# Kernel tuning notes

Hardware: AMD Instinct MI355X
Metric: run time of the kernel (lower is better)

Reference implementation:

```python
import jax, jax.numpy as jnp
import numpy as np

K = 512          # num_embeddings
D = 8            # latent_dim
DECAY = 0.99     # ema_decay
EPS = 1e-5


def setup_inputs() -> dict:
    key = jax.random.key(0)
    k1, k2 = jax.random.split(key)
    z = jax.random.normal(k1, (64, D, 64, 64), dtype=jnp.float32)
    # codebook initialized uniform(-1/K, 1/K) as in the torch module
    codebook = jax.random.uniform(k2, (K, D), dtype=jnp.float32,
                                  minval=-1.0 / K, maxval=1.0 / K)
    ema_cluster_size = jnp.zeros((K,), dtype=jnp.float32)
    ema_w = jnp.zeros((K, D), dtype=jnp.float32)
    return {"z": z, "codebook": codebook,
            "ema_cluster_size": ema_cluster_size, "ema_w": ema_w}


def reference(z, codebook, ema_cluster_size, ema_w):
    B, C, H, W = z.shape
    # (B, HW, C) flattened latents, matching z.view(B,C,-1).permute(0,2,1)
    flat = z.reshape(B, C, H * W).transpose(0, 2, 1)

    # cdist p=2: ||z||^2 - 2 z.e + ||e||^2, then sqrt (argmin unaffected,
    # but we keep the sqrt for faithfulness to torch.cdist)
    z_sq = jnp.sum(flat * flat, axis=-1, keepdims=True)        # (B, N, 1)
    e_sq = jnp.sum(codebook * codebook, axis=-1)               # (K,)
    dots = jnp.einsum('bnd,kd->bnk', flat, codebook)           # (B, N, K)
    distances = jnp.sqrt(jnp.maximum(z_sq - 2.0 * dots + e_sq, 0.0))

    indices = jnp.argmin(distances, axis=-1)                   # (B, N) int

    # embedding gather with the OLD codebook (as in the torch forward)
    z_q = codebook[indices]                                    # (B, N, D)
    z_q = z_q.transpose(0, 2, 1).reshape(B, C, H, W)

    commitment_loss = jnp.mean((jax.lax.stop_gradient(z_q) - z) ** 2)
    loss = commitment_loss  # use_ema=True branch

    # ---- EMA in-place codebook update (buffers) ----
    idx_flat = indices.reshape(-1)                             # (B*N,)
    inp_flat = flat.reshape(-1, C)                             # (B*N, D)
    counts = jax.ops.segment_sum(jnp.ones_like(idx_flat, dtype=z.dtype),
                                 idx_flat, num_segments=K)     # (K,)
    sums = jax.ops.segment_sum(inp_flat, idx_flat, num_segments=K)  # (K, D)

    new_cs = ema_cluster_size * DECAY + counts * (1.0 - DECAY)
    new_w = ema_w * DECAY + sums * (1.0 - DECAY)
    n = jnp.sum(new_cs)
    cs_smoothed = (new_cs + EPS) / (n + K * EPS) * n
    new_codebook = new_w / cs_smoothed[:, None]

    return z_q, loss, new_codebook, cs_smoothed, new_w
```

## Files before the change

kernel.cpp:

```cpp
#include <hip/hip_runtime.h>

constexpr int Kc   = 512;
constexpr int Dc   = 8;
constexpr int HWc  = 4096;
constexpr int CHWc = Dc * HWc;
constexpr int Mc   = 64 * HWc;
constexpr int TOTALc = Mc * Dc;

constexpr int REP      = 8;
constexpr int RSTRIDE  = 4616;
constexpr int ACC_FLOATS = REP * RSTRIDE;

typedef float v2f __attribute__((ext_vector_type(2)));

__global__ __launch_bounds__(256) void vq_prep(const float* __restrict__ cb,
                                               float* __restrict__ ws) {
    const int tid = blockIdx.x * 256 + threadIdx.x;
    float4* w4 = (float4*)ws;
    for (int i = tid; i < ACC_FLOATS / 4; i += gridDim.x * 256)
        w4[i] = float4{0.f, 0.f, 0.f, 0.f};
    if (blockIdx.x == 0) {
        for (int k = threadIdx.x; k < Kc; k += 256) {
            float s = 0.f;
#pragma unroll
            for (int c = 0; c < Dc; ++c) {
                const float e = cb[k * Dc + c];
                s = fmaf(e, e, s);
            }
            ws[ACC_FLOATS + k] = s;
        }
    }
}

__global__ __launch_bounds__(512, 8) void vq_main(const float* __restrict__ z,
                                                  const float* __restrict__ cb,
                                                  const float* __restrict__ esq,
                                                  float* __restrict__ ws,
                                                  float* __restrict__ zq) {
    __shared__ float s_mn[8][256];
    __shared__ int   s_im[8][256];
    __shared__ float s_counts[Kc];
    __shared__ float s_sums[Kc * Dc];
    __shared__ float s_loss;

    const int t = threadIdx.x;
    for (int i = t; i < Kc; i += 512) s_counts[i] = 0.f;
    for (int i = t; i < Kc * Dc; i += 512) s_sums[i] = 0.f;
    if (t == 0) s_loss = 0.f;

    const int l = t & 63;
    const int g  = __builtin_amdgcn_readfirstlane(t >> 6);
    const int k0 = g << 6;

    const int base = blockIdx.x * 256;
    const int b  = base >> 12;
    const int n0 = (base & (HWc - 1)) + l;
    const float* zb = z + b * CHWc + n0;

    v2f zzA[Dc], zzB[Dc];
#pragma unroll
    for (int c = 0; c < Dc; ++c) {
        zzA[c] = v2f{-2.0f * zb[c * HWc],       -2.0f * zb[c * HWc + 64]};
        zzB[c] = v2f{-2.0f * zb[c * HWc + 128], -2.0f * zb[c * HWc + 192]};
    }

    const unsigned long long* cbq = (const unsigned long long*)cb;

    float mn0 = 3.4e38f, mn1 = 3.4e38f, mn2 = 3.4e38f, mn3 = 3.4e38f;
    int   i0 = k0, i1 = k0, i2 = k0, i3 = k0;
#pragma unroll 2
    for (int kk = 0; kk < 64; ++kk) {
        const int k = k0 + kk;
        const unsigned long long q0 = cbq[4 * k + 0];
        const unsigned long long q1 = cbq[4 * k + 1];
        const unsigned long long q2 = cbq[4 * k + 2];
        const unsigned long long q3 = cbq[4 * k + 3];
        const float ev = esq[k];
        v2f aA = {ev, ev};
        v2f aB = {ev, ev};
#define PKSTEP(Q, P0, P1)                                              \
        asm("v_pk_fma_f32 %0, %2, %4, %0 op_sel_hi:[1,0,1]\n\t"        \
            "v_pk_fma_f32 %1, %3, %4, %1 op_sel_hi:[1,0,1]\n\t"        \
            "v_pk_fma_f32 %0, %5, %4, %0 op_sel:[0,1,0]\n\t"           \
            "v_pk_fma_f32 %1, %6, %4, %1 op_sel:[0,1,0]"               \
            : "+v"(aA), "+v"(aB)                                       \
            : "v"(zzA[P0]), "v"(zzB[P0]), "s"(Q), "v"(zzA[P1]), "v"(zzB[P1]))
        PKSTEP(q0, 0, 1);
        PKSTEP(q1, 2, 3);
        PKSTEP(q2, 4, 5);
        PKSTEP(q3, 6, 7);
#undef PKSTEP
        const float a0 = aA.x, a1 = aA.y, a2 = aB.x, a3 = aB.y;
        bool c;
        c = a0 < mn0; mn0 = c ? a0 : mn0; i0 = c ? k : i0;
        c = a1 < mn1; mn1 = c ? a1 : mn1; i1 = c ? k : i1;
        c = a2 < mn2; mn2 = c ? a2 : mn2; i2 = c ? k : i2;
        c = a3 < mn3; mn3 = c ? a3 : mn3; i3 = c ? k : i3;
    }
    s_mn[g][l]       = mn0;  s_im[g][l]       = i0;
    s_mn[g][l +  64] = mn1;  s_im[g][l +  64] = i1;
    s_mn[g][l + 128] = mn2;  s_im[g][l + 128] = i2;
    s_mn[g][l + 192] = mn3;  s_im[g][l + 192] = i3;
    __syncthreads();

    if (t < 256) {
        const int v = t;
        float mn = s_mn[0][v];
        int   im = s_im[0][v];
#pragma unroll
        for (int gg = 1; gg < 8; ++gg) {
            const float m2 = s_mn[gg][v];
            const int   j2 = s_im[gg][v];
            const bool  c2 = m2 < mn;
            mn = c2 ? m2 : mn;
            im = c2 ? j2 : im;
        }

        const float4* cb4 = (const float4*)cb;
        const float4 qa = cb4[im * 2], qb = cb4[im * 2 + 1];
        const float q[Dc] = {qa.x, qa.y, qa.z, qa.w, qb.x, qb.y, qb.z, qb.w};

        const int nv = (base & (HWc - 1)) + v;
        const float* zv = z + b * CHWc + nv;
        float* zqv = zq + b * CHWc + nv;
        float lsum = 0.f;
        float zr[Dc];
#pragma unroll
        for (int c = 0; c < Dc; ++c) {
            zr[c] = zv[c * HWc];
            zqv[c * HWc] = q[c];
            const float d = q[c] - zr[c];
            lsum = fmaf(d, d, lsum);
        }

        unsafeAtomicAdd(&s_counts[im], 1.0f);
#pragma unroll
        for (int c = 0; c < Dc; ++c)
            unsafeAtomicAdd(&s_sums[im * Dc + c], zr[c]);
        unsafeAtomicAdd(&s_loss, lsum);
    }
    __syncthreads();

    float* acc = ws + (blockIdx.x & (REP - 1)) * RSTRIDE;
    for (int i = t; i < Kc; i += 512) {
        const float val = s_counts[i];
        if (val != 0.f) unsafeAtomicAdd(&acc[i], val);
    }
    for (int i = t; i < Kc * Dc; i += 512) {
        const float val = s_sums[i];
        if (val != 0.f) unsafeAtomicAdd(&acc[512 + i], val);
    }
    if (t == 0) unsafeAtomicAdd(&acc[4608], s_loss);
}

__global__ __launch_bounds__(512) void vq_final(const float* __restrict__ ws,
                                                const float* __restrict__ ema_cs,
                                                const float* __restrict__ ema_w,
                                                float* __restrict__ out) {
    constexpr float DEC  = 0.99f;
    constexpr float OMD  = (float)(1.0 - 0.99);
    constexpr float EPSf = 1e-5f;
    constexpr float KEPS = (float)(512 * 1e-5);
    __shared__ float red[512];
    __shared__ float s_cs[512];

    const int t = threadIdx.x;
    float cnt = 0.f;
#pragma unroll
    for (int r = 0; r < REP; ++r) cnt += ws[r * RSTRIDE + t];
    const float ncs = ema_cs[t] * DEC + cnt * OMD;
    red[t] = ncs;
    __syncthreads();
    for (int s = 256; s > 0; s >>= 1) {
        if (t < s) red[t] += red[t + s];
        __syncthreads();
    }
    const float n  = red[0];
    const float cs = (ncs + EPSf) / (n + KEPS) * n;
    s_cs[t] = cs;

    float* out_loss = out + TOTALc;
    float* out_cb   = out + TOTALc + 1;
    float* out_cs   = out_cb + Kc * Dc;
    float* out_nw   = out_cs + Kc;

    __syncthreads();

    const int blk = blockIdx.x;
    if (blk == 0) {
        out_cs[t] = cs;
        if (t == 0) {
            float ls = 0.f;
#pragma unroll
            for (int r = 0; r < REP; ++r) ls += ws[r * RSTRIDE + 4608];
            out_loss[0] = ls * (1.0f / 2097152.0f);
        }
    } else {
        const int e = (blk - 1) * 512 + t;
        float sm = 0.f;
#pragma unroll
        for (int r = 0; r < REP; ++r) sm += ws[r * RSTRIDE + 512 + e];
        const float nw = ema_w[e] * DEC + sm * OMD;
        out_nw[e] = nw;
        out_cb[e] = nw / s_cs[e >> 3];
    }
}

extern "C" void kernel_launch(void* const* d_in, const int* in_sizes, int n_in,
                              void* d_out, int out_size, void* d_ws, size_t ws_size,
                              hipStream_t stream) {
    const float* z      = (const float*)d_in[0];
    const float* cb     = (const float*)d_in[1];
    const float* ema_cs = (const float*)d_in[2];
    const float* ema_w  = (const float*)d_in[3];
    float* out = (float*)d_out;
    float* ws  = (float*)d_ws;

    vq_prep<<<32, 256, 0, stream>>>(cb, ws);
    vq_main<<<Mc / 256, 512, 0, stream>>>(z, cb, ws + ACC_FLOATS, ws, out);
    vq_final<<<9, 512, 0, stream>>>(ws, ema_cs, ema_w, out);
}
```

Before: 109.6 us.

## Fuse final EMA reduction into main kernel via last-block ticket counter

Removes the separate vq_final launch. Each main block bumps a global ticket counter after flushing its partial sums, and the last block to arrive does the EMA finalisation. The first FMA step now seeds the accumulators from the squared-norm term directly, and the codebook loop unroll goes from 2 to 4. This saves a kernel launch and its gap, at the cost of a device-scope atomic and fence per block and a serialized tail done by a single block.

```diff
diff --git a/kernel.cpp b/kernel.cpp
--- a/kernel.cpp
+++ b/kernel.cpp
@@ -29,6 +29,8 @@
             }
             ws[ACC_FLOATS + k] = s;
         }
+        if (threadIdx.x == 0)
+            ((unsigned*)ws)[ACC_FLOATS + 512] = 0u;
     }
 }
 
@@ -36,12 +38,16 @@
                                                   const float* __restrict__ cb,
                                                   const float* __restrict__ esq,
                                                   float* __restrict__ ws,
-                                                  float* __restrict__ zq) {
+                                                  float* __restrict__ zq,
+                                                  const float* __restrict__ ema_cs,
+                                                  const float* __restrict__ ema_w,
+                                                  float* __restrict__ out) {
     __shared__ float s_mn[8][256];
     __shared__ int   s_im[8][256];
     __shared__ float s_counts[Kc];
     __shared__ float s_sums[Kc * Dc];
     __shared__ float s_loss;
+    __shared__ unsigned s_tick;
 
     const int t = threadIdx.x;
     for (int i = t; i < Kc; i += 512) s_counts[i] = 0.f;
@@ -68,7 +74,7 @@
 
     float mn0 = 3.4e38f, mn1 = 3.4e38f, mn2 = 3.4e38f, mn3 = 3.4e38f;
     int   i0 = k0, i1 = k0, i2 = k0, i3 = k0;
-#pragma unroll 2
+#pragma unroll 4
     for (int kk = 0; kk < 64; ++kk) {
         const int k = k0 + kk;
         const unsigned long long q0 = cbq[4 * k + 0];
@@ -76,8 +82,15 @@
         const unsigned long long q2 = cbq[4 * k + 2];
         const unsigned long long q3 = cbq[4 * k + 3];
         const float ev = esq[k];
-        v2f aA = {ev, ev};
-        v2f aB = {ev, ev};
+        const v2f vev2 = {ev, ev};
+        v2f aA, aB;
+        asm("v_pk_fma_f32 %0, %2, %4, %5 op_sel_hi:[1,0,1]\n\t"
+            "v_pk_fma_f32 %1, %3, %4, %5 op_sel_hi:[1,0,1]\n\t"
+            "v_pk_fma_f32 %0, %6, %4, %0 op_sel:[0,1,0]\n\t"
+            "v_pk_fma_f32 %1, %7, %4, %1 op_sel:[0,1,0]"
+            : "=&v"(aA), "=&v"(aB)
+            : "v"(zzA[0]), "v"(zzB[0]), "s"(q0), "v"(vev2),
+              "v"(zzA[1]), "v"(zzB[1]));
 #define PKSTEP(Q, P0, P1)                                              \
         asm("v_pk_fma_f32 %0, %2, %4, %0 op_sel_hi:[1,0,1]\n\t"        \
             "v_pk_fma_f32 %1, %3, %4, %1 op_sel_hi:[1,0,1]\n\t"        \
@@ -85,7 +98,6 @@
             "v_pk_fma_f32 %1, %6, %4, %1 op_sel:[0,1,0]"               \
             : "+v"(aA), "+v"(aB)                                       \
             : "v"(zzA[P0]), "v"(zzB[P0]), "s"(Q), "v"(zzA[P1]), "v"(zzB[P1]))
-        PKSTEP(q0, 0, 1);
         PKSTEP(q1, 2, 3);
         PKSTEP(q2, 4, 5);
         PKSTEP(q3, 6, 7);
@@ -151,58 +163,59 @@
         if (val != 0.f) unsafeAtomicAdd(&acc[512 + i], val);
     }
     if (t == 0) unsafeAtomicAdd(&acc[4608], s_loss);
-}
-
-__global__ __launch_bounds__(512) void vq_final(const float* __restrict__ ws,
-                                                const float* __restrict__ ema_cs,
-                                                const float* __restrict__ ema_w,
-                                                float* __restrict__ out) {
-    constexpr float DEC  = 0.99f;
-    constexpr float OMD  = (float)(1.0 - 0.99);
-    constexpr float EPSf = 1e-5f;
-    constexpr float KEPS = (float)(512 * 1e-5);
-    __shared__ float red[512];
-    __shared__ float s_cs[512];
-
-    const int t = threadIdx.x;
-    float cnt = 0.f;
-#pragma unroll
-    for (int r = 0; r < REP; ++r) cnt += ws[r * RSTRIDE + t];
-    const float ncs = ema_cs[t] * DEC + cnt * OMD;
-    red[t] = ncs;
-    __syncthreads();
-    for (int s = 256; s > 0; s >>= 1) {
-        if (t < s) red[t] += red[t + s];
+
+    __threadfence();
+    __syncthreads();
+    if (t == 0)
+        s_tick = __hip_atomic_fetch_add((unsigned*)(ws + ACC_FLOATS + 512), 1u,
+                                        __ATOMIC_ACQ_REL,
+                                        __HIP_MEMORY_SCOPE_AGENT);
+    __syncthreads();
+    if (s_tick == 1023u) {
+        __threadfence();
+        constexpr float DEC  = 0.99f;
+        constexpr float OMD  = (float)(1.0 - 0.99);
+        constexpr float EPSf = 1e-5f;
+        constexpr float KEPS = (float)(512 * 1e-5);
+        float* red = s_counts;
+        float* scs = &s_mn[0][0];
+
+        float cnt = 0.f;
+#pragma unroll
+        for (int r = 0; r < REP; ++r) cnt += ws[r * RSTRIDE + t];
+        const float ncs = ema_cs[t] * DEC + cnt * OMD;
+        red[t] = ncs;
         __syncthreads();
-    }
-    const float n  = red[0];
-    const float cs = (ncs + EPSf) / (n + KEPS) * n;
-    s_cs[t] = cs;
-
-    float* out_loss = out + TOTALc;
-    float* out_cb   = out + TOTALc + 1;
-    float* out_cs   = out_cb + Kc * Dc;
-    float* out_nw   = out_cs + Kc;
-
-    __syncthreads();
-
-    const int blk = blockIdx.x;
-    if (blk == 0) {
+        for (int s = 256; s > 0; s >>= 1) {
+            if (t < s) red[t] += red[t + s];
+            __syncthreads();
+        }
+        const float n  = red[0];
+        const float cs = (ncs + EPSf) / (n + KEPS) * n;
+        scs[t] = cs;
+
+        float* out_loss = out + TOTALc;
+        float* out_cb   = out + TOTALc + 1;
+        float* out_cs   = out_cb + Kc * Dc;
+        float* out_nw   = out_cs + Kc;
+
         out_cs[t] = cs;
+        __syncthreads();
+
+        for (int e = t; e < Kc * Dc; e += 512) {
+            float sm = 0.f;
+#pragma unroll
+            for (int r = 0; r < REP; ++r) sm += ws[r * RSTRIDE + 512 + e];
+            const float nw = ema_w[e] * DEC + sm * OMD;
+            out_nw[e] = nw;
+            out_cb[e] = nw / scs[e >> 3];
+        }
         if (t == 0) {
             float ls = 0.f;
 #pragma unroll
             for (int r = 0; r < REP; ++r) ls += ws[r * RSTRIDE + 4608];
             out_loss[0] = ls * (1.0f / 2097152.0f);
         }
-    } else {
-        const int e = (blk - 1) * 512 + t;
-        float sm = 0.f;
-#pragma unroll
-        for (int r = 0; r < REP; ++r) sm += ws[r * RSTRIDE + 512 + e];
-        const float nw = ema_w[e] * DEC + sm * OMD;
-        out_nw[e] = nw;
-        out_cb[e] = nw / s_cs[e >> 3];
     }
 }
 
@@ -217,6 +230,6 @@
     float* ws  = (float*)d_ws;
 
     vq_prep<<<32, 256, 0, stream>>>(cb, ws);
-    vq_main<<<Mc / 256, 512, 0, stream>>>(z, cb, ws + ACC_FLOATS, ws, out);
-    vq_final<<<9, 512, 0, stream>>>(ws, ema_cs, ema_w, out);
+    vq_main<<<Mc / 256, 512, 0, stream>>>(z, cb, ws + ACC_FLOATS, ws, out,
+                                          ema_cs, ema_w, out);
 }
```

Result: slower. 242.0 us (+120.9%).
